# Kernel tuning notes

Measured on AMD Instinct MI355X. Metric: run time of the kernel, lower is better.

## Reference

```python
import jax, jax.numpy as jnp
import numpy as np

N_NODES = 1_000_000
N_EDGES = 32_000_000


def setup_inputs() -> dict:
    key = jax.random.key(0)
    k_x, k_e, k_w1, k_w2 = jax.random.split(key, 4)
    x = jax.random.normal(k_x, (N_NODES, 2), dtype=jnp.float32)
    edge_index = jax.random.randint(k_e, (2, N_EDGES), 0, N_NODES, dtype=jnp.int64)
    # Glorot-ish init for the tiny GCN weights
    W1 = jax.random.normal(k_w1, (2, 8), dtype=jnp.float32) * 0.5
    b1 = jnp.zeros((8,), dtype=jnp.float32)
    W2 = jax.random.normal(k_w2, (8, 1), dtype=jnp.float32) * 0.3
    b2 = jnp.zeros((1,), dtype=jnp.float32)
    return {"x": x, "edge_index": edge_index, "W1": W1, "b1": b1, "W2": W2, "b2": b2}


def _gcn_conv(x, src, dst, norm, W, b, n_nodes):
    # PyG GCNConv: h = x @ W; out[i] = sum_{j->i} norm_e * h[j]; out += b
    h = x @ W                                   # [N, out_dim]
    msg = h[src] * norm[:, None]                # gather over edges (incl. self-loops)
    out = jax.ops.segment_sum(msg, dst, num_segments=n_nodes)
    return out + b


def _norm_and_loops(edge_index, n_nodes, dtype):
    # Add self-loops, compute symmetric normalization deg^{-1/2}[src]*deg^{-1/2}[dst]
    loop = jnp.arange(n_nodes, dtype=edge_index.dtype)
    src = jnp.concatenate([edge_index[0], loop])
    dst = jnp.concatenate([edge_index[1], loop])
    deg = jax.ops.segment_sum(jnp.ones_like(dst, dtype=dtype), dst, num_segments=n_nodes)
    dinv = jnp.where(deg > 0, jax.lax.rsqrt(jnp.maximum(deg, 1.0)), 0.0).astype(dtype)
    norm = dinv[src] * dinv[dst]                # [E + N]
    return src, dst, norm


def reference(x, edge_index, W1, b1, W2, b2):
    n_nodes = x.shape[0]
    src, dst, norm = _norm_and_loops(edge_index, n_nodes, x.dtype)
    h = _gcn_conv(x, src, dst, norm, W1, b1, n_nodes)
    h = jax.nn.relu(h)
    h = _gcn_conv(h, src, dst, norm, W2, b2, n_nodes)
    return jax.nn.sigmoid(h)                    # [N, 1]
```

## Files before the change

kernel.cpp:

```cpp
#include <hip/hip_runtime.h>

#define NN 1000000
#define NE 32000000
#define SCAN_B 256

#define BK_SH 11
#define BK_SZ 2048
#define NB 489
#define GAB 512
#define CHUNK 62500
#define NL (NB * GAB)
#define NBS (NL / SCAN_B)
#define TILE 8192
#define CB 512

typedef int vi4 __attribute__((ext_vector_type(4)));

__global__ void detect_kernel(const int* __restrict__ ei, int* __restrict__ flag) {
    __shared__ int nz;
    if (threadIdx.x == 0) nz = 0;
    __syncthreads();
    int w = ei[2 * threadIdx.x + 1];
    if (w != 0) atomicAdd(&nz, 1);
    __syncthreads();
    if (threadIdx.x == 0) *flag = (nz == 0) ? 1 : 0;
}

__global__ void passA_kernel(const int* __restrict__ ei, int* __restrict__ hist,
                             const int* __restrict__ flagp, int nE) {
    __shared__ int h[NB];
    int t = threadIdx.x;
    for (int b = t; b < NB; b += 512) h[b] = 0;
    __syncthreads();
    int shift = *flagp;
    int start = blockIdx.x * CHUNK;
    int end = min(start + CHUNK, nE);
    if (shift == 0) {
        const int* dstp = ei + nE;
        for (int i = start + (t << 2); i < end; i += 2048) {
            vi4 d = __builtin_nontemporal_load((const vi4*)(dstp + i));
            atomicAdd(&h[d.x >> BK_SH], 1);
            atomicAdd(&h[d.y >> BK_SH], 1);
            atomicAdd(&h[d.z >> BK_SH], 1);
            atomicAdd(&h[d.w >> BK_SH], 1);
        }
    } else {
        const int* dstp = ei + ((size_t)nE << 1);
        for (int i = start + t; i < end; i += 512) {
            int d = __builtin_nontemporal_load(dstp + ((size_t)i << 1));
            atomicAdd(&h[d >> BK_SH], 1);
        }
    }
    __syncthreads();
    for (int b = t; b < NB; b += 512)
        hist[(size_t)b * GAB + blockIdx.x] = h[b];
}

__global__ void scan1_kernel(int* __restrict__ data, int* __restrict__ bsum, int n) {
    __shared__ int sm[SCAN_B];
    int t = threadIdx.x;
    int i = blockIdx.x * SCAN_B + t;
    int v = (i < n) ? data[i] : 0;
    sm[t] = v;
    __syncthreads();
    for (int o = 1; o < SCAN_B; o <<= 1) {
        int a = (t >= o) ? sm[t - o] : 0;
        __syncthreads();
        sm[t] += a;
        __syncthreads();
    }
    if (i < n) data[i] = sm[t] - v;
    if (t == SCAN_B - 1) bsum[blockIdx.x] = sm[t];
}

__global__ void scan2_kernel(int* __restrict__ bsum, int nb) {
    __shared__ int sm[1024];
    int t = threadIdx.x;
    int base = t * 4;
    int v[4];
    int s = 0;
#pragma unroll
    for (int j = 0; j < 4; ++j) {
        v[j] = (base + j < nb) ? bsum[base + j] : 0;
        s += v[j];
    }
    sm[t] = s;
    __syncthreads();
    for (int o = 1; o < 1024; o <<= 1) {
        int a = (t >= o) ? sm[t - o] : 0;
        __syncthreads();
        sm[t] += a;
        __syncthreads();
    }
    int run = sm[t] - s;
#pragma unroll
    for (int j = 0; j < 4; ++j) {
        if (base + j < nb) bsum[base + j] = run;
        run += v[j];
    }
}

__global__ void __launch_bounds__(CB, 2)
passC_kernel(const int* __restrict__ ei, const int* __restrict__ hist,
             const int* __restrict__ bsum, unsigned int* __restrict__ pairs,
             const int* __restrict__ flagp, int nE) {
    __shared__ int cnt[NB];
    __shared__ int scn[NB];
    __shared__ int off[NB];
    __shared__ int curb[NB];
    __shared__ int ssum[CB];
    __shared__ unsigned int stg[TILE];
    __shared__ unsigned short bkt[TILE];

    int t = threadIdx.x;
    for (int b = t; b < NB; b += CB) {
        int flat = b * GAB + blockIdx.x;
        curb[b] = hist[flat] + bsum[flat >> 8];
        cnt[b] = 0;
    }
    __syncthreads();
    int shift = *flagp;
    int start = blockIdx.x * CHUNK;
    int end = min(start + CHUNK, nE);
    const int* srcp = ei;
    const int* dstp = ei + nE;

    for (int ts = start; ts < end; ts += TILE) {
        int te = min(ts + TILE, end);
        int tn = te - ts;
        if (shift == 0) {
            for (int i = ts + (t << 2); i + 4 <= te; i += (CB << 2)) {
                vi4 d = *(const vi4*)(dstp + i);
                atomicAdd(&cnt[d.x >> BK_SH], 1);
                atomicAdd(&cnt[d.y >> BK_SH], 1);
                atomicAdd(&cnt[d.z >> BK_SH], 1);
                atomicAdd(&cnt[d.w >> BK_SH], 1);
            }
        } else {
            for (int i = ts + t; i < te; i += CB) {
                int d = ei[((size_t)(nE + i)) << 1];
                atomicAdd(&cnt[d >> BK_SH], 1);
            }
        }
        __syncthreads();
        {
            int v = (t < NB) ? cnt[t] : 0;
            ssum[t] = v;
            __syncthreads();
            for (int o = 1; o < CB; o <<= 1) {
                int a = (t >= o) ? ssum[t - o] : 0;
                __syncthreads();
                ssum[t] += a;
                __syncthreads();
            }
            if (t < NB) { scn[t] = ssum[t] - v; off[t] = 0; }
        }
        __syncthreads();
        if (shift == 0) {
            for (int i = ts + (t << 2); i + 4 <= te; i += (CB << 2)) {
                vi4 s = *(const vi4*)(srcp + i);
                vi4 d = *(const vi4*)(dstp + i);
                int b, pos;
                b = d.x >> BK_SH; pos = scn[b] + atomicAdd(&off[b], 1);
                stg[pos] = (unsigned)s.x | ((unsigned)(d.x & (BK_SZ - 1)) << 20);
                bkt[pos] = (unsigned short)b;
                b = d.y >> BK_SH; pos = scn[b] + atomicAdd(&off[b], 1);
                stg[pos] = (unsigned)s.y | ((unsigned)(d.y & (BK_SZ - 1)) << 20);
                bkt[pos] = (unsigned short)b;
                b = d.z >> BK_SH; pos = scn[b] + atomicAdd(&off[b], 1);
                stg[pos] = (unsigned)s.z | ((unsigned)(d.z & (BK_SZ - 1)) << 20);
                bkt[pos] = (unsigned short)b;
                b = d.w >> BK_SH; pos = scn[b] + atomicAdd(&off[b], 1);
                stg[pos] = (unsigned)s.w | ((unsigned)(d.w & (BK_SZ - 1)) << 20);
                bkt[pos] = (unsigned short)b;
            }
        } else {
            for (int i = ts + t; i < te; i += CB) {
                int s = ei[(size_t)i << 1];
                int d = ei[((size_t)(nE + i)) << 1];
                int b = d >> BK_SH;
                int pos = scn[b] + atomicAdd(&off[b], 1);
                stg[pos] = (unsigned)s | ((unsigned)(d & (BK_SZ - 1)) << 20);
                bkt[pos] = (unsigned short)b;
            }
        }
        __syncthreads();
        for (int j = t; j < tn; j += CB) {
            int b = bkt[j];
            pairs[curb[b] + (j - scn[b])] = stg[j];
        }
        __syncthreads();
        for (int b = t; b < NB; b += CB) {
            curb[b] += cnt[b];
            cnt[b] = 0;
        }
        __syncthreads();
    }
}

__device__ __forceinline__ void bucket_range(const int* __restrict__ hist,
                                             const int* __restrict__ bsum,
                                             int b, int nE, int& base, int& endp) {
    int f0 = b * GAB;
    base = hist[f0] + bsum[f0 >> 8];
    if (b + 1 < NB) {
        int f1 = (b + 1) * GAB;
        endp = hist[f1] + bsum[f1 >> 8];
    } else {
        endp = nE;
    }
}

__device__ __forceinline__ void aligned_range(int base, int endp, int& abase, int& rend) {
    abase = (base + 3) & ~3;
    if (abase > endp) abase = endp;
    rend = abase + ((endp - abase) & ~3);
}

__global__ void passD0_kernel(const unsigned int* __restrict__ pairs,
                              const int* __restrict__ hist, const int* __restrict__ bsum,
                              const float2* __restrict__ x,
                              float* __restrict__ dinv, float2* __restrict__ xd,
                              int nE, int nN) {
    __shared__ int degl[BK_SZ];
    int t = threadIdx.x;
    int b = blockIdx.x;
    for (int j = t; j < BK_SZ; j += 1024) degl[j] = 0;
    __syncthreads();
    int base, endp, abase, rend;
    bucket_range(hist, bsum, b, nE, base, endp);
    aligned_range(base, endp, abase, rend);
    {
        int k = base + t;
        if (k < abase) atomicAdd(&degl[pairs[k] >> 20], 1);
        int k2 = rend + t;
        if (k2 < endp) atomicAdd(&degl[pairs[k2] >> 20], 1);
    }
    for (int k = abase + (t << 2); k + 4 <= rend; k += 4096) {
        vi4 q = *(const vi4*)(pairs + k);
        atomicAdd(&degl[(unsigned)q.x >> 20], 1);
        atomicAdd(&degl[(unsigned)q.y >> 20], 1);
        atomicAdd(&degl[(unsigned)q.z >> 20], 1);
        atomicAdd(&degl[(unsigned)q.w >> 20], 1);
    }
    __syncthreads();
    for (int j = t; j < BK_SZ; j += 1024) {
        int nid = (b << BK_SH) + j;
        if (nid < nN) {
            float di = rsqrtf((float)(degl[j] + 1));
            dinv[nid] = di;
            float2 v = x[nid];
            xd[nid] = make_float2(v.x * di, v.y * di);
        }
    }
}

__global__ void passL1_kernel(const unsigned int* __restrict__ pairs,
                              const int* __restrict__ hist, const int* __restrict__ bsum,
                              const float* __restrict__ dinv, const float2* __restrict__ xd,
                              const float* __restrict__ W1, const float* __restrict__ b1,
                              const float* __restrict__ W2,
                              float* __restrict__ hd, int nE, int nN) {
    __shared__ float ax[BK_SZ];
    __shared__ float ay[BK_SZ];
    int t = threadIdx.x;
    int b = blockIdx.x;
    for (int j = t; j < BK_SZ; j += 1024) { ax[j] = 0.f; ay[j] = 0.f; }
    __syncthreads();
    int base, endp, abase, rend;
    bucket_range(hist, bsum, b, nE, base, endp);
    aligned_range(base, endp, abase, rend);
    {
        int k = base + t;
        if (k < abase) {
            unsigned int p = pairs[k];
            float2 v = xd[p & 0xFFFFF];
            atomicAdd(&ax[p >> 20], v.x);
            atomicAdd(&ay[p >> 20], v.y);
        }
        int k2 = rend + t;
        if (k2 < endp) {
            unsigned int p = pairs[k2];
            float2 v = xd[p & 0xFFFFF];
            atomicAdd(&ax[p >> 20], v.x);
            atomicAdd(&ay[p >> 20], v.y);
        }
    }
    for (int k = abase + (t << 2); k + 4 <= rend; k += 4096) {
        vi4 q = *(const vi4*)(pairs + k);
        unsigned int p[4] = {(unsigned)q.x, (unsigned)q.y, (unsigned)q.z, (unsigned)q.w};
        float2 v[4];
#pragma unroll
        for (int j = 0; j < 4; ++j) v[j] = xd[p[j] & 0xFFFFF];
#pragma unroll
        for (int j = 0; j < 4; ++j) {
            int dl = p[j] >> 20;
            atomicAdd(&ax[dl], v[j].x);
            atomicAdd(&ay[dl], v[j].y);
        }
    }
    __syncthreads();
    for (int j = t; j < BK_SZ; j += 1024) {
        int nid = (b << BK_SH) + j;
        if (nid < nN) {
            float dd = dinv[nid];
            float2 xs = xd[nid];
            float AX = (ax[j] + xs.x * dd) * dd;
            float AY = (ay[j] + xs.y * dd) * dd;
            float acc = 0.f;
#pragma unroll
            for (int c = 0; c < 8; ++c) {
                float h = fmaf(AX, W1[c], fmaf(AY, W1[8 + c], b1[c]));
                acc = fmaf(fmaxf(h, 0.f), W2[c], acc);
            }
            hd[nid] = acc * dd;
        }
    }
}

__global__ void passL2_kernel(const unsigned int* __restrict__ pairs,
                              const int* __restrict__ hist, const int* __restrict__ bsum,
                              const float* __restrict__ dinv, const float* __restrict__ hd,
                              const float* __restrict__ b2,
                              float* __restrict__ out, int nE, int nN) {
    __shared__ float ag[BK_SZ];
    int t = threadIdx.x;
    int b = blockIdx.x;
    for (int j = t; j < BK_SZ; j += 1024) ag[j] = 0.f;
    __syncthreads();
    int base, endp, abase, rend;
    bucket_range(hist, bsum, b, nE, base, endp);
    aligned_range(base, endp, abase, rend);
    {
        int k = base + t;
        if (k < abase) {
            unsigned int p = pairs[k];
            atomicAdd(&ag[p >> 20], hd[p & 0xFFFFF]);
        }
        int k2 = rend + t;
        if (k2 < endp) {
            unsigned int p = pairs[k2];
            atomicAdd(&ag[p >> 20], hd[p & 0xFFFFF]);
        }
    }
    for (int k = abase + (t << 2); k + 4 <= rend; k += 4096) {
        vi4 q = *(const vi4*)(pairs + k);
        unsigned int p[4] = {(unsigned)q.x, (unsigned)q.y, (unsigned)q.z, (unsigned)q.w};
        float v[4];
#pragma unroll
        for (int j = 0; j < 4; ++j) v[j] = hd[p[j] & 0xFFFFF];
#pragma unroll
        for (int j = 0; j < 4; ++j) atomicAdd(&ag[p[j] >> 20], v[j]);
    }
    __syncthreads();
    for (int j = t; j < BK_SZ; j += 1024) {
        int nid = (b << BK_SH) + j;
        if (nid < nN) {
            float z = fmaf(dinv[nid], ag[j] + hd[nid], b2[0]);
            out[nid] = 1.f / (1.f + expf(-z));
        }
    }
}


__global__ void deg_kernel(const int* __restrict__ ei, int* __restrict__ deg,
                           const int* __restrict__ flagp, int nE) {
    int i = blockIdx.x * blockDim.x + threadIdx.x;
    if (i >= nE) return;
    int shift = *flagp;
    int d = ei[((size_t)nE << shift) + ((size_t)i << shift)];
    atomicAdd(&deg[d], 1);
}

__global__ void prep_kernel(const int* __restrict__ deg, const float2* __restrict__ x,
                            float* __restrict__ dinv, float2* __restrict__ xd, int nN) {
    int i = blockIdx.x * blockDim.x + threadIdx.x;
    if (i >= nN) return;
    float di = rsqrtf((float)(deg[i] + 1));
    dinv[i] = di;
    float2 v = x[i];
    xd[i] = make_float2(v.x * di, v.y * di);
}

__device__ __forceinline__ void load_edge(const int* __restrict__ ei, int shift,
                                          int nE, int i, int& s, int& d) {
    s = ei[(size_t)i << shift];
    d = ei[((size_t)nE << shift) + ((size_t)i << shift)];
}

__global__ void l1a_kernel(const int* __restrict__ ei, const float2* __restrict__ xd,
                           float* __restrict__ agg, const int* __restrict__ flagp, int nE) {
    int i = blockIdx.x * blockDim.x + threadIdx.x;
    if (i >= nE) return;
    int shift = *flagp;
    int s, d;
    load_edge(ei, shift, nE, i, s, d);
    float2 v = xd[s];
    unsafeAtomicAdd(&agg[(size_t)d * 2], v.x);
    unsafeAtomicAdd(&agg[(size_t)d * 2 + 1], v.y);
}

__global__ void h2f_kernel(const float2* __restrict__ agg, const float2* __restrict__ xd,
                           const float* __restrict__ dinv, const float* __restrict__ W1,
                           const float* __restrict__ b1, const float* __restrict__ W2,
                           float* __restrict__ hd, int nN) {
    int d = blockIdx.x * blockDim.x + threadIdx.x;
    if (d >= nN) return;
    float dd = dinv[d];
    float2 a = agg[d];
    float2 xs = xd[d];
    float ax = (a.x + xs.x * dd) * dd;
    float ay = (a.y + xs.y * dd) * dd;
    float acc = 0.f;
#pragma unroll
    for (int j = 0; j < 8; ++j) {
        float h = fmaf(ax, W1[j], fmaf(ay, W1[8 + j], b1[j]));
        acc = fmaf(fmaxf(h, 0.f), W2[j], acc);
    }
    hd[d] = acc * dd;
}

__global__ void l2a_kernel(const int* __restrict__ ei, const float* __restrict__ hd,
                           float* __restrict__ out2, const int* __restrict__ flagp, int nE) {
    int i = blockIdx.x * blockDim.x + threadIdx.x;
    if (i >= nE) return;
    int shift = *flagp;
    int s, d;
    load_edge(ei, shift, nE, i, s, d);
    unsafeAtomicAdd(&out2[d], hd[s]);
}

__global__ void finf_kernel(const float* __restrict__ out2, const float* __restrict__ hd,
                            const float* __restrict__ dinv, const float* __restrict__ b2,
                            float* __restrict__ out, int nN) {
    int d = blockIdx.x * blockDim.x + threadIdx.x;
    if (d >= nN) return;
    float z = fmaf(dinv[d], out2[d] + hd[d], b2[0]);
    out[d] = 1.f / (1.f + expf(-z));
}

extern "C" void kernel_launch(void* const* d_in, const int* in_sizes, int n_in,
                              void* d_out, int out_size, void* d_ws, size_t ws_size,
                              hipStream_t stream) {
    const float* x  = (const float*)d_in[0];
    const int*   ei = (const int*)d_in[1];
    const float* W1 = (const float*)d_in[2];
    const float* b1 = (const float*)d_in[3];
    const float* W2 = (const float*)d_in[4];
    const float* b2 = (const float*)d_in[5];
    float* out = (float*)d_out;

    const int nE = NE, nN = NN;
    const int bs = 256;
    char* ws = (char*)d_ws;
    const size_t MiB = 1 << 20;

    const size_t csr_need = 18 * MiB + (size_t)nE * 4;

    if (ws_size >= csr_need) {
        int*          hist  = (int*)ws;
        int*          bsum  = (int*)(ws + 1 * MiB);
        int*          flag  = (int*)(ws + 1 * MiB + 65536);
        float*        dinv  = (float*)(ws + 2 * MiB);
        float2*       xd    = (float2*)(ws + 6 * MiB);
        float*        hd    = (float*)(ws + 14 * MiB);
        unsigned int* pairs = (unsigned int*)(ws + 18 * MiB);

        detect_kernel<<<1, 256, 0, stream>>>(ei, flag);
        passA_kernel<<<GAB, 512, 0, stream>>>(ei, hist, flag, nE);
        scan1_kernel<<<NBS, SCAN_B, 0, stream>>>(hist, bsum, NL);
        scan2_kernel<<<1, 1024, 0, stream>>>(bsum, NBS);
        passC_kernel<<<GAB, CB, 0, stream>>>(ei, hist, bsum, pairs, flag, nE);
        passD0_kernel<<<NB, 1024, 0, stream>>>(pairs, hist, bsum, (const float2*)x,
                                               dinv, xd, nE, nN);
        passL1_kernel<<<NB, 1024, 0, stream>>>(pairs, hist, bsum, dinv, xd,
                                               W1, b1, W2, hd, nE, nN);
        passL2_kernel<<<NB, 1024, 0, stream>>>(pairs, hist, bsum, dinv, hd,
                                               b2, out, nE, nN);
    } else {
        int*    deg  = (int*)ws;
        float*  agg  = (float*)(ws + 4 * MiB);
        float*  out2 = (float*)(ws + 12 * MiB);
        float*  dinv = (float*)(ws + 16 * MiB);
        float2* xd   = (float2*)(ws + 20 * MiB);
        float*  hd   = (float*)(ws + 28 * MiB);
        int*    flag = (int*)(ws + 32 * MiB);

        hipMemsetAsync(ws, 0, 16 * MiB, stream);

        detect_kernel<<<1, 256, 0, stream>>>(ei, flag);
        deg_kernel<<<(nE + bs - 1) / bs, bs, 0, stream>>>(ei, deg, flag, nE);
        prep_kernel<<<(nN + bs - 1) / bs, bs, 0, stream>>>(deg, (const float2*)x, dinv, xd, nN);
        l1a_kernel<<<(nE + bs - 1) / bs, bs, 0, stream>>>(ei, xd, agg, flag, nE);
        h2f_kernel<<<(nN + bs - 1) / bs, bs, 0, stream>>>((const float2*)agg, xd, dinv,
                                                          W1, b1, W2, hd, nN);
        l2a_kernel<<<(nE + bs - 1) / bs, bs, 0, stream>>>(ei, hd, out2, flag, nE);
        finf_kernel<<<(nN + bs - 1) / bs, bs, 0, stream>>>(out2, hd, dinv, b2, out, nN);
    }
}
```

Before: 1.026 ms.

## Register-cache dst loads across passes, vectorize int64 reads, use wave-shuffle tile scan

The bucket-scatter pass now keeps each thread's destination vectors in registers between the counting and scatter phases, so dst is read from global memory once per tile instead of twice. Int64 edge indices are read as 128-bit vectors covering two elements, in both the histogram and the scatter kernels. The per-tile shared-memory Hillis-Steele scan with many barriers is replaced by a wavefront shuffle scan plus a small cross-wave scan. The cost is higher register pressure from the cached vectors under the two-blocks-per-CU launch bound.

```diff
diff --git a/kernel.cpp b/kernel.cpp
--- a/kernel.cpp
+++ b/kernel.cpp
@@ -46,9 +46,10 @@
         }
     } else {
         const int* dstp = ei + ((size_t)nE << 1);
-        for (int i = start + t; i < end; i += 512) {
-            int d = __builtin_nontemporal_load(dstp + ((size_t)i << 1));
-            atomicAdd(&h[d >> BK_SH], 1);
+        for (int i = start + (t << 1); i < end; i += 1024) {
+            vi4 d2 = __builtin_nontemporal_load((const vi4*)(dstp + ((size_t)i << 1)));
+            atomicAdd(&h[d2.x >> BK_SH], 1);
+            atomicAdd(&h[d2.z >> BK_SH], 1);
         }
     }
     __syncthreads();
@@ -98,6 +99,33 @@
         if (base + j < nb) bsum[base + j] = run;
         run += v[j];
     }
+}
+
+__device__ __forceinline__ void tile_scan(int t, int lane, int wid,
+                                          int* __restrict__ cnt, int* __restrict__ scn,
+                                          int* __restrict__ off, int* __restrict__ wsum) {
+    int v = (t < NB) ? cnt[t] : 0;
+    int sw = v;
+#pragma unroll
+    for (int o = 1; o < 64; o <<= 1) {
+        int n = __shfl_up(sw, o, 64);
+        if (lane >= o) sw += n;
+    }
+    if (lane == 63) wsum[wid] = sw;
+    __syncthreads();
+    if (t < 8) {
+        int w = wsum[t];
+        int iw = w;
+#pragma unroll
+        for (int o = 1; o < 8; o <<= 1) {
+            int n = __shfl_up(iw, o, 8);
+            if (t >= o) iw += n;
+        }
+        wsum[t] = iw - w;
+    }
+    __syncthreads();
+    if (t < NB) { scn[t] = wsum[wid] + sw - v; off[t] = 0; }
+    __syncthreads();
 }
 
 __global__ void __launch_bounds__(CB, 2)
@@ -108,11 +136,12 @@
     __shared__ int scn[NB];
     __shared__ int off[NB];
     __shared__ int curb[NB];
-    __shared__ int ssum[CB];
+    __shared__ int wsum[8];
     __shared__ unsigned int stg[TILE];
     __shared__ unsigned short bkt[TILE];
 
     int t = threadIdx.x;
+    int lane = t & 63, wid = t >> 6;
     for (int b = t; b < NB; b += CB) {
         int flat = b * GAB + blockIdx.x;
         curb[b] = hist[flat] + bsum[flat >> 8];
@@ -122,79 +151,95 @@
     int shift = *flagp;
     int start = blockIdx.x * CHUNK;
     int end = min(start + CHUNK, nE);
-    const int* srcp = ei;
-    const int* dstp = ei + nE;
-
-    for (int ts = start; ts < end; ts += TILE) {
-        int te = min(ts + TILE, end);
-        int tn = te - ts;
-        if (shift == 0) {
-            for (int i = ts + (t << 2); i + 4 <= te; i += (CB << 2)) {
-                vi4 d = *(const vi4*)(dstp + i);
-                atomicAdd(&cnt[d.x >> BK_SH], 1);
-                atomicAdd(&cnt[d.y >> BK_SH], 1);
-                atomicAdd(&cnt[d.z >> BK_SH], 1);
-                atomicAdd(&cnt[d.w >> BK_SH], 1);
-            }
-        } else {
-            for (int i = ts + t; i < te; i += CB) {
-                int d = ei[((size_t)(nE + i)) << 1];
-                atomicAdd(&cnt[d >> BK_SH], 1);
-            }
-        }
-        __syncthreads();
-        {
-            int v = (t < NB) ? cnt[t] : 0;
-            ssum[t] = v;
-            __syncthreads();
-            for (int o = 1; o < CB; o <<= 1) {
-                int a = (t >= o) ? ssum[t - o] : 0;
-                __syncthreads();
-                ssum[t] += a;
-                __syncthreads();
-            }
-            if (t < NB) { scn[t] = ssum[t] - v; off[t] = 0; }
-        }
-        __syncthreads();
-        if (shift == 0) {
-            for (int i = ts + (t << 2); i + 4 <= te; i += (CB << 2)) {
-                vi4 s = *(const vi4*)(srcp + i);
-                vi4 d = *(const vi4*)(dstp + i);
-                int b, pos;
-                b = d.x >> BK_SH; pos = scn[b] + atomicAdd(&off[b], 1);
-                stg[pos] = (unsigned)s.x | ((unsigned)(d.x & (BK_SZ - 1)) << 20);
-                bkt[pos] = (unsigned short)b;
-                b = d.y >> BK_SH; pos = scn[b] + atomicAdd(&off[b], 1);
-                stg[pos] = (unsigned)s.y | ((unsigned)(d.y & (BK_SZ - 1)) << 20);
-                bkt[pos] = (unsigned short)b;
-                b = d.z >> BK_SH; pos = scn[b] + atomicAdd(&off[b], 1);
-                stg[pos] = (unsigned)s.z | ((unsigned)(d.z & (BK_SZ - 1)) << 20);
-                bkt[pos] = (unsigned short)b;
-                b = d.w >> BK_SH; pos = scn[b] + atomicAdd(&off[b], 1);
-                stg[pos] = (unsigned)s.w | ((unsigned)(d.w & (BK_SZ - 1)) << 20);
-                bkt[pos] = (unsigned short)b;
-            }
-        } else {
-            for (int i = ts + t; i < te; i += CB) {
-                int s = ei[(size_t)i << 1];
-                int d = ei[((size_t)(nE + i)) << 1];
-                int b = d >> BK_SH;
-                int pos = scn[b] + atomicAdd(&off[b], 1);
-                stg[pos] = (unsigned)s | ((unsigned)(d & (BK_SZ - 1)) << 20);
-                bkt[pos] = (unsigned short)b;
-            }
-        }
-        __syncthreads();
-        for (int j = t; j < tn; j += CB) {
-            int b = bkt[j];
-            pairs[curb[b] + (j - scn[b])] = stg[j];
-        }
-        __syncthreads();
-        for (int b = t; b < NB; b += CB) {
-            curb[b] += cnt[b];
-            cnt[b] = 0;
-        }
-        __syncthreads();
+
+    if (shift == 1) {
+        const size_t dbase = (size_t)nE << 1;
+        for (int ts = start; ts < end; ts += TILE) {
+            int te = min(ts + TILE, end);
+            int tn = te - ts;
+            vi4 dd[8];
+#pragma unroll
+            for (int q = 0; q < 8; ++q) {
+                int i = ts + (t << 1) + (q << 10);
+                if (i + 2 <= te) {
+                    dd[q] = __builtin_nontemporal_load(
+                        (const vi4*)(ei + dbase + ((size_t)i << 1)));
+                    atomicAdd(&cnt[dd[q].x >> BK_SH], 1);
+                    atomicAdd(&cnt[dd[q].z >> BK_SH], 1);
+                }
+            }
+            __syncthreads();
+            tile_scan(t, lane, wid, cnt, scn, off, wsum);
+#pragma unroll
+            for (int q = 0; q < 8; ++q) {
+                int i = ts + (t << 1) + (q << 10);
+                if (i + 2 <= te) {
+                    vi4 ss = __builtin_nontemporal_load(
+                        (const vi4*)(ei + ((size_t)i << 1)));
+                    int b0 = dd[q].x >> BK_SH;
+                    int pos = scn[b0] + atomicAdd(&off[b0], 1);
+                    stg[pos] = (unsigned)ss.x | ((unsigned)(dd[q].x & (BK_SZ - 1)) << 20);
+                    bkt[pos] = (unsigned short)b0;
+                    int b1 = dd[q].z >> BK_SH;
+                    pos = scn[b1] + atomicAdd(&off[b1], 1);
+                    stg[pos] = (unsigned)ss.z | ((unsigned)(dd[q].z & (BK_SZ - 1)) << 20);
+                    bkt[pos] = (unsigned short)b1;
+                }
+            }
+            __syncthreads();
+            for (int j = t; j < tn; j += CB) {
+                int b = bkt[j];
+                pairs[curb[b] + (j - scn[b])] = stg[j];
+            }
+            __syncthreads();
+            for (int b = t; b < NB; b += CB) { curb[b] += cnt[b]; cnt[b] = 0; }
+            __syncthreads();
+        }
+    } else {
+        const int* srcp = ei;
+        const int* dstp = ei + nE;
+        for (int ts = start; ts < end; ts += TILE) {
+            int te = min(ts + TILE, end);
+            int tn = te - ts;
+            vi4 dd[4];
+#pragma unroll
+            for (int q = 0; q < 4; ++q) {
+                int i = ts + (t << 2) + (q << 11);
+                if (i + 4 <= te) {
+                    dd[q] = __builtin_nontemporal_load((const vi4*)(dstp + i));
+                    atomicAdd(&cnt[dd[q].x >> BK_SH], 1);
+                    atomicAdd(&cnt[dd[q].y >> BK_SH], 1);
+                    atomicAdd(&cnt[dd[q].z >> BK_SH], 1);
+                    atomicAdd(&cnt[dd[q].w >> BK_SH], 1);
+                }
+            }
+            __syncthreads();
+            tile_scan(t, lane, wid, cnt, scn, off, wsum);
+#pragma unroll
+            for (int q = 0; q < 4; ++q) {
+                int i = ts + (t << 2) + (q << 11);
+                if (i + 4 <= te) {
+                    vi4 ss = __builtin_nontemporal_load((const vi4*)(srcp + i));
+                    int dv[4] = {dd[q].x, dd[q].y, dd[q].z, dd[q].w};
+                    int sv[4] = {ss.x, ss.y, ss.z, ss.w};
+#pragma unroll
+                    for (int e = 0; e < 4; ++e) {
+                        int b = dv[e] >> BK_SH;
+                        int pos = scn[b] + atomicAdd(&off[b], 1);
+                        stg[pos] = (unsigned)sv[e] | ((unsigned)(dv[e] & (BK_SZ - 1)) << 20);
+                        bkt[pos] = (unsigned short)b;
+                    }
+                }
+            }
+            __syncthreads();
+            for (int j = t; j < tn; j += CB) {
+                int b = bkt[j];
+                pairs[curb[b] + (j - scn[b])] = stg[j];
+            }
+            __syncthreads();
+            for (int b = t; b < NB; b += CB) { curb[b] += cnt[b]; cnt[b] = 0; }
+            __syncthreads();
+        }
     }
 }
 
```

Measured after the change: 997.4 us, median of 2. -2.8%, faster.
